# Kernel optimization log

Hardware: AMD Instinct MI355X
Metric: run time of the kernel (lower is better)

The kernel has to match this reference:

```python
import jax, jax.numpy as jnp
import numpy as np

STRIDE = 1
PADDING = 1
THRESHOLD = 0.5
NAN_FRAC = 0.05


def _conv(x, k, stride):
    return jax.lax.conv_general_dilated(
        x, k, (stride, stride), 'VALID',
        dimension_numbers=('NCHW', 'OIHW', 'NCHW'))


def setup_inputs() -> dict:
    key = jax.random.key(0)
    k1, k2, k3, k4 = jax.random.split(key, 4)
    B, C, H, W = 16, 128, 128, 128
    OC, KH, KW = 256, 3, 3
    x = jax.random.normal(k1, (B, C, H, W), jnp.float32)
    nan_mask = jax.random.uniform(k2, (B, C, H, W)) < NAN_FRAC
    x = jnp.where(nan_mask, jnp.nan, x)
    kernel = jax.random.normal(k3, (OC, C, KH, KW), jnp.float32) * 0.05
    bias = jax.random.normal(k4, (OC,), jnp.float32) * 0.05
    return {"x": x, "kernel": kernel, "bias": bias}


def reference(x, kernel, bias):
    # NaN-aware conv: per-patch nan stats shared across out_channels.
    p = PADDING
    x = jnp.pad(x, ((0, 0), (0, 0), (p, p), (p, p)))  # zero pad (zeros are valid values)
    mask = jnp.isnan(x)
    x0 = jnp.where(mask, jnp.zeros((), x.dtype), x)
    OC, C, KH, KW = kernel.shape
    total = float(C * KH * KW)
    ones = jnp.ones((1, C, KH, KW), x.dtype)
    maskf = mask.astype(x.dtype)
    nan_count = _conv(maskf, ones, STRIDE)      # [B,1,oh,ow]
    val_sum = _conv(x0, ones, STRIDE)           # sum of non-nan values per patch
    valid = total - nan_count
    patch_mean = val_sum / jnp.maximum(valid, 1.0)
    s1 = _conv(x0, kernel, STRIDE)              # conv with NaNs zeroed
    m = _conv(maskf, kernel, STRIDE)            # sum of kernel weights at NaN positions
    out = s1 + patch_mean * m + bias[None, :, None, None]
    bad = nan_count / total >= THRESHOLD        # includes all-NaN patches
    return jnp.where(bad, jnp.nan, out)
```

## Files before the change

kernel.cpp:

```cpp
#include <hip/hip_runtime.h>


typedef __attribute__((ext_vector_type(8))) short bf16x8;
typedef __attribute__((ext_vector_type(4))) float f32x4;

#define HH 128
#define WW 128
#define CC 128

__device__ __forceinline__ unsigned short f2bf(float f) {
    union { float f; unsigned int i; } v; v.f = f;
    unsigned int u = v.i;
    if ((u & 0x7FFFFFFFu) > 0x7F800000u) return (unsigned short)((u >> 16) | 0x0040u);
    unsigned int r = u + 0x7FFFu + ((u >> 16) & 1u);
    return (unsigned short)(r >> 16);
}
__device__ __forceinline__ unsigned int sel2(unsigned int v, unsigned int pmu) {
    unsigned int lo = v & 0xFFFFu, hi = v >> 16;
    if ((lo & 0x7FFFu) > 0x7F80u) lo = pmu;
    if ((hi & 0x7FFFu) > 0x7F80u) hi = pmu;
    return lo | (hi << 16);
}
__device__ __forceinline__ void gl16(const void* g, void* l) {
    __builtin_amdgcn_global_load_lds(
        (const __attribute__((address_space(1))) unsigned int*)g,
        (__attribute__((address_space(3))) unsigned int*)l, 16, 0, 0);
}

__global__ void k_transpose_stats(const float* __restrict__ x,
                                  unsigned short* __restrict__ xT,
                                  float* __restrict__ cnt,
                                  float* __restrict__ sum, int b0) {
    int bh = blockIdx.x;
    int bl = bh >> 7, h = bh & 127;
    int b = b0 + bl;
    int w = threadIdx.x;
    const float* xp = x + ((long)b * CC * HH * WW) + h * WW + w;
    unsigned short* xTp = xT + ((((long)bh << 7) + w) << 7);
    int cntv = 0; float sumv = 0.f;
    for (int c8 = 0; c8 < 16; ++c8) {
        unsigned short s8[8];
        #pragma unroll
        for (int j = 0; j < 8; ++j) {
            float fv = xp[(long)(c8 * 8 + j) * (HH * WW)];
            unsigned int bits = __float_as_uint(fv);
            if ((bits & 0x7FFFFFFFu) > 0x7F800000u) { cntv++; s8[j] = 0x7FC0u; }
            else { sumv += fv; s8[j] = f2bf(fv); }
        }
        uint4 p;
        p.x = (unsigned)s8[0] | ((unsigned)s8[1] << 16);
        p.y = (unsigned)s8[2] | ((unsigned)s8[3] << 16);
        p.z = (unsigned)s8[4] | ((unsigned)s8[5] << 16);
        p.w = (unsigned)s8[6] | ((unsigned)s8[7] << 16);
        *(uint4*)(xTp + c8 * 8) = p;
    }
    cnt[(bh << 7) + w] = (float)cntv;
    sum[(bh << 7) + w] = sumv;
}

__global__ void k_patchmean(const float* __restrict__ cnt, const float* __restrict__ sum,
                            unsigned short* __restrict__ pm) {
    int idx = blockIdx.x * 256 + threadIdx.x;
    int ow = idx & 127, oh = (idx >> 7) & 127, bl = idx >> 14;
    float nc = 0.f, vs = 0.f;
    #pragma unroll
    for (int kh = 0; kh < 3; ++kh) {
        int ih = oh + kh - 1; if (ih < 0 || ih >= HH) continue;
        #pragma unroll
        for (int kw = 0; kw < 3; ++kw) {
            int iw = ow + kw - 1; if (iw < 0 || iw >= WW) continue;
            int p = (((bl << 7) + ih) << 7) + iw;
            nc += cnt[p]; vs += sum[p];
        }
    }
    float pmv = vs / fmaxf(1152.f - nc, 1.f);
    unsigned short r = f2bf(pmv);
    if (nc >= 576.f) r = 0x7FC0u;
    pm[idx] = r;
}

__global__ void k_w2(const float* __restrict__ krn, unsigned short* __restrict__ W2) {
    int e = blockIdx.x * 256 + threadIdx.x;
    int s = e & 63;
    int r = (e >> 6) & 255;
    int half = (e >> 14) & 1;
    int khw = e >> 15;
    int c = (half << 6) | (s ^ ((r & 7) << 3));
    W2[e] = f2bf(krn[(r * 128 + c) * 9 + khw]);
}

__global__ __launch_bounds__(256) void k_gemm(
    const unsigned short* __restrict__ xT, const unsigned short* __restrict__ pm,
    const unsigned short* __restrict__ W2, const float* __restrict__ bias,
    float* __restrict__ out, int b0) {
    __shared__ __align__(16) unsigned short lA[2][64 * 64];
    __shared__ __align__(16) unsigned short lB[2][256 * 64];

    int bid = blockIdx.x;
    int ow0 = (bid & 1) << 6;
    int oh  = (bid >> 1) & 127;
    int bl  = bid >> 8;
    int b   = b0 + bl;

    int tid = threadIdx.x;
    int lane = tid & 63, wave = tid >> 6;
    int l15 = lane & 15, quad = lane >> 4;

    int arow = tid >> 2, apart = tid & 3;
    int ow = ow0 + arow;
    unsigned int pmr = pm[(((bl << 7) + oh) << 7) + ow];

    const char* w2base = (const char*)W2;
    int bgoff = (wave << 13) + (lane << 4);
    int bloff = (wave << 13);

    f32x4 acc[4][4];
    #pragma unroll
    for (int i = 0; i < 4; ++i)
        #pragma unroll
        for (int j = 0; j < 4; ++j) acc[i][j] = (f32x4)0.f;

    auto STAGE = [&](unsigned short* la, unsigned short* lb, int s) {
        int khw = s >> 1, c0 = (s & 1) << 6;
        int kh = khw / 3, kw = khw - kh * 3;
        int ih = oh + kh - 1, iw = ow + kw - 1;
        const char* bsrc = w2base + (s << 15) + bgoff;
        char* ldst = (char*)lb + bloff;
        #pragma unroll
        for (int i = 0; i < 8; ++i)
            gl16(bsrc + (i << 10), ldst + (i << 10));
        uint4 v0 = {0u,0u,0u,0u}, v1 = {0u,0u,0u,0u};
        if ((unsigned)ih < 128u && (unsigned)iw < 128u) {
            const unsigned short* ap =
                xT + ((((long)((bl << 7) + ih) << 7) + iw) << 7) + c0 + (apart << 4);
            v0 = *(const uint4*)ap;
            v1 = *(const uint4*)(ap + 8);
        }
        uint4 r0, r1;
        r0.x = sel2(v0.x, pmr); r0.y = sel2(v0.y, pmr);
        r0.z = sel2(v0.z, pmr); r0.w = sel2(v0.w, pmr);
        r1.x = sel2(v1.x, pmr); r1.y = sel2(v1.y, pmr);
        r1.z = sel2(v1.z, pmr); r1.w = sel2(v1.w, pmr);
        char* lar = (char*)la + (arow << 7);
        int sw = (arow & 7) << 4;
        *(uint4*)(lar + (((apart << 5) | 0)  ^ sw)) = r0;
        *(uint4*)(lar + (((apart << 5) | 16) ^ sw)) = r1;
    };

    auto COMPUTE = [&](const unsigned short* la, const unsigned short* lb) {
        int swr = (l15 & 7) << 4;
        #pragma unroll
        for (int ks = 0; ks < 2; ++ks) {
            bf16x8 af[4], bfr[4];
            int cb = ((ks << 6) | (quad << 4)) ^ swr;
            #pragma unroll
            for (int mi = 0; mi < 4; ++mi) {
                int r = (mi << 4) + l15;
                af[mi] = *(const bf16x8*)((const char*)la + (r << 7) + cb);
            }
            #pragma unroll
            for (int ni = 0; ni < 4; ++ni) {
                int r = (wave << 6) + (ni << 4) + l15;
                bfr[ni] = *(const bf16x8*)((const char*)lb + (r << 7) + cb);
            }
            #pragma unroll
            for (int mi = 0; mi < 4; ++mi)
                #pragma unroll
                for (int ni = 0; ni < 4; ++ni)
                    acc[mi][ni] = __builtin_amdgcn_mfma_f32_16x16x32_bf16(
                        af[mi], bfr[ni], acc[mi][ni], 0, 0, 0);
        }
    };

    STAGE(lA[0], lB[0], 0);
    __syncthreads();
    for (int s = 0; s < 18; s += 2) {
        STAGE(lA[1], lB[1], s + 1);
        COMPUTE(lA[0], lB[0]);
        __syncthreads();
        if (s + 2 < 18) STAGE(lA[0], lB[0], s + 2);
        COMPUTE(lA[1], lB[1]);
        __syncthreads();
    }

    #pragma unroll
    for (int ni = 0; ni < 4; ++ni) {
        int oc = (wave << 6) + (ni << 4) + l15;
        float bv = bias[oc];
        float* op = out + ((long)((b << 8) + oc) * 128 + oh) * 128 + ow0;
        #pragma unroll
        for (int mi = 0; mi < 4; ++mi) {
            int og = (mi << 4) + (quad << 2);
            float4 o;
            o.x = acc[mi][ni][0] + bv;
            o.y = acc[mi][ni][1] + bv;
            o.z = acc[mi][ni][2] + bv;
            o.w = acc[mi][ni][3] + bv;
            *(float4*)(op + og) = o;
        }
    }
}

extern "C" void kernel_launch(void* const* d_in, const int* in_sizes, int n_in,
                              void* d_out, int out_size, void* d_ws, size_t ws_size,
                              hipStream_t stream) {
    const float* x    = (const float*)d_in[0];
    const float* krn  = (const float*)d_in[1];
    const float* bias = (const float*)d_in[2];
    float* out = (float*)d_out;

    const size_t W2_BYTES = 294912ull * 2;
    int G = 16;
    while (G > 1) {
        size_t need = W2_BYTES + 256
                    + (size_t)G * (16384ull * 128 * 2)
                    + (size_t)G * (16384ull * 4) * 2
                    + (size_t)G * (16384ull * 2)
                    + 1024;
        if (need <= ws_size) break;
        G >>= 1;
    }

    char* ws = (char*)d_ws;
    size_t off = 0;
    auto carve = [&](size_t bytes) { char* p = ws + off; off += (bytes + 255) & ~255ull; return p; };
    unsigned short* W2  = (unsigned short*)carve(W2_BYTES);
    unsigned short* xT  = (unsigned short*)carve((size_t)G * 16384 * 128 * 2);
    float*          cnt = (float*)carve((size_t)G * 16384 * 4);
    float*          sum = (float*)carve((size_t)G * 16384 * 4);
    unsigned short* pm  = (unsigned short*)carve((size_t)G * 16384 * 2);

    k_w2<<<dim3(1152), dim3(256), 0, stream>>>(krn, W2);
    for (int b0 = 0; b0 < 16; b0 += G) {
        k_transpose_stats<<<dim3(G * 128), dim3(128), 0, stream>>>(x, xT, cnt, sum, b0);
        k_patchmean<<<dim3(G * 64), dim3(256), 0, stream>>>(cnt, sum, pm);
        k_gemm<<<dim3(G * 256), dim3(256), 0, stream>>>(xT, pm, W2, bias, out, b0);
    }
}
```

Baseline: 672.9 us.

## Enlarge GEMM tile to full row, software-pipeline loads, coalesce transpose writes via LDS

```diff
diff --git a/kernel.cpp b/kernel.cpp
--- a/kernel.cpp
+++ b/kernel.cpp
@@ -26,17 +26,18 @@
         (const __attribute__((address_space(1))) unsigned int*)g,
         (__attribute__((address_space(3))) unsigned int*)l, 16, 0, 0);
 }
+#define SBAR() __builtin_amdgcn_sched_barrier(0)
 
 __global__ void k_transpose_stats(const float* __restrict__ x,
                                   unsigned short* __restrict__ xT,
                                   float* __restrict__ cnt,
                                   float* __restrict__ sum, int b0) {
+    __shared__ __align__(16) unsigned short ls[128][136];
     int bh = blockIdx.x;
     int bl = bh >> 7, h = bh & 127;
     int b = b0 + bl;
     int w = threadIdx.x;
     const float* xp = x + ((long)b * CC * HH * WW) + h * WW + w;
-    unsigned short* xTp = xT + ((((long)bh << 7) + w) << 7);
     int cntv = 0; float sumv = 0.f;
     for (int c8 = 0; c8 < 16; ++c8) {
         unsigned short s8[8];
@@ -52,10 +53,18 @@
         p.y = (unsigned)s8[2] | ((unsigned)s8[3] << 16);
         p.z = (unsigned)s8[4] | ((unsigned)s8[5] << 16);
         p.w = (unsigned)s8[6] | ((unsigned)s8[7] << 16);
-        *(uint4*)(xTp + c8 * 8) = p;
+        *(uint4*)&ls[w][c8 * 8] = p;
     }
     cnt[(bh << 7) + w] = (float)cntv;
     sum[(bh << 7) + w] = sumv;
+    __syncthreads();
+    unsigned short* xb = xT + ((long)bh << 14);
+    int ch = w & 15, pw = w >> 4;
+    #pragma unroll
+    for (int r = 0; r < 16; ++r) {
+        int p = (r << 3) + pw;
+        *(uint4*)(xb + (p << 7) + (ch << 3)) = *(const uint4*)&ls[p][ch << 3];
+    }
 }
 
 __global__ void k_patchmean(const float* __restrict__ cnt, const float* __restrict__ sum,
@@ -89,30 +98,28 @@
     W2[e] = f2bf(krn[(r * 128 + c) * 9 + khw]);
 }
 
-__global__ __launch_bounds__(256) void k_gemm(
+__global__ __launch_bounds__(512, 2) void k_gemm(
     const unsigned short* __restrict__ xT, const unsigned short* __restrict__ pm,
     const unsigned short* __restrict__ W2, const float* __restrict__ bias,
     float* __restrict__ out, int b0) {
-    __shared__ __align__(16) unsigned short lA[2][64 * 64];
+    __shared__ __align__(16) unsigned short lA[2][128 * 64];
     __shared__ __align__(16) unsigned short lB[2][256 * 64];
 
     int bid = blockIdx.x;
-    int ow0 = (bid & 1) << 6;
-    int oh  = (bid >> 1) & 127;
-    int bl  = bid >> 8;
-    int b   = b0 + bl;
+    int oh = bid & 127, bl = bid >> 7;
+    int b = b0 + bl;
 
     int tid = threadIdx.x;
     int lane = tid & 63, wave = tid >> 6;
+    int wm = wave >> 2, wn = wave & 3;
     int l15 = lane & 15, quad = lane >> 4;
 
     int arow = tid >> 2, apart = tid & 3;
-    int ow = ow0 + arow;
-    unsigned int pmr = pm[(((bl << 7) + oh) << 7) + ow];
+    unsigned int pmr = pm[(((bl << 7) + oh) << 7) + arow];
 
     const char* w2base = (const char*)W2;
-    int bgoff = (wave << 13) + (lane << 4);
-    int bloff = (wave << 13);
+    int bsrcoff = (wave << 10) + (lane << 4);
+    int bdstoff = (wave << 10);
 
     f32x4 acc[4][4];
     #pragma unroll
@@ -120,22 +127,29 @@
         #pragma unroll
         for (int j = 0; j < 4; ++j) acc[i][j] = (f32x4)0.f;
 
-    auto STAGE = [&](unsigned short* la, unsigned short* lb, int s) {
-        int khw = s >> 1, c0 = (s & 1) << 6;
+    auto issueB = [&](int s, unsigned short* lbbuf) {
+        const char* src = w2base + ((long)s << 15) + bsrcoff;
+        char* dst = (char*)lbbuf + bdstoff;
+        #pragma unroll
+        for (int i = 0; i < 4; ++i)
+            gl16(src + (i << 13), dst + (i << 13));
+    };
+    auto loadA = [&](int s, uint4& v0, uint4& v1, unsigned& msk) {
+        int khw = s >> 1, c0s = (s & 1) << 6;
         int kh = khw / 3, kw = khw - kh * 3;
-        int ih = oh + kh - 1, iw = ow + kw - 1;
-        const char* bsrc = w2base + (s << 15) + bgoff;
-        char* ldst = (char*)lb + bloff;
-        #pragma unroll
-        for (int i = 0; i < 8; ++i)
-            gl16(bsrc + (i << 10), ldst + (i << 10));
-        uint4 v0 = {0u,0u,0u,0u}, v1 = {0u,0u,0u,0u};
-        if ((unsigned)ih < 128u && (unsigned)iw < 128u) {
-            const unsigned short* ap =
-                xT + ((((long)((bl << 7) + ih) << 7) + iw) << 7) + c0 + (apart << 4);
-            v0 = *(const uint4*)ap;
-            v1 = *(const uint4*)(ap + 8);
-        }
+        int ih = oh + kh - 1, iw = arow + kw - 1;
+        bool valid = ((unsigned)ih < 128u) && ((unsigned)iw < 128u);
+        int ihc = ih < 0 ? 0 : (ih > 127 ? 127 : ih);
+        int iwc = iw < 0 ? 0 : (iw > 127 ? 127 : iw);
+        const uint4* ap = (const uint4*)(xT +
+            ((((long)((bl << 7) + ihc) << 7) + iwc) << 7) + c0s + (apart << 4));
+        v0 = ap[0];
+        v1 = ap[1];
+        msk = valid ? 0xFFFFFFFFu : 0u;
+    };
+    auto stageA = [&](uint4 v0, uint4 v1, unsigned msk, unsigned short* la) {
+        v0.x &= msk; v0.y &= msk; v0.z &= msk; v0.w &= msk;
+        v1.x &= msk; v1.y &= msk; v1.z &= msk; v1.w &= msk;
         uint4 r0, r1;
         r0.x = sel2(v0.x, pmr); r0.y = sel2(v0.y, pmr);
         r0.z = sel2(v0.z, pmr); r0.w = sel2(v0.w, pmr);
@@ -146,7 +160,6 @@
         *(uint4*)(lar + (((apart << 5) | 0)  ^ sw)) = r0;
         *(uint4*)(lar + (((apart << 5) | 16) ^ sw)) = r1;
     };
-
     auto COMPUTE = [&](const unsigned short* la, const unsigned short* lb) {
         int swr = (l15 & 7) << 4;
         #pragma unroll
@@ -155,12 +168,12 @@
             int cb = ((ks << 6) | (quad << 4)) ^ swr;
             #pragma unroll
             for (int mi = 0; mi < 4; ++mi) {
-                int r = (mi << 4) + l15;
+                int r = (wm << 6) + (mi << 4) + l15;
                 af[mi] = *(const bf16x8*)((const char*)la + (r << 7) + cb);
             }
             #pragma unroll
             for (int ni = 0; ni < 4; ++ni) {
-                int r = (wave << 6) + (ni << 4) + l15;
+                int r = (wn << 6) + (ni << 4) + l15;
                 bfr[ni] = *(const bf16x8*)((const char*)lb + (r << 7) + cb);
             }
             #pragma unroll
@@ -172,31 +185,52 @@
         }
     };
 
-    STAGE(lA[0], lB[0], 0);
-    __syncthreads();
-    for (int s = 0; s < 18; s += 2) {
-        STAGE(lA[1], lB[1], s + 1);
-        COMPUTE(lA[0], lB[0]);
-        __syncthreads();
-        if (s + 2 < 18) STAGE(lA[0], lB[0], s + 2);
-        COMPUTE(lA[1], lB[1]);
-        __syncthreads();
+    uint4 av0[2], av1[2]; unsigned am[2];
+
+    issueB(0, lB[0]); SBAR();
+    loadA(0, av0[0], av1[0], am[0]); SBAR();
+    loadA(1, av0[1], av1[1], am[1]); SBAR();
+    asm volatile("s_waitcnt vmcnt(2)" ::: "memory");
+    SBAR();
+    stageA(av0[0], av1[0], am[0], lA[0]);
+    asm volatile("s_waitcnt lgkmcnt(0)" ::: "memory");
+    SBAR();
+    __builtin_amdgcn_s_barrier();
+    SBAR();
+
+    #pragma unroll
+    for (int s = 0; s < 18; ++s) {
+        const int cur = s & 1, nxt = cur ^ 1;
+        if (s < 17) { issueB(s + 1, lB[nxt]); SBAR(); }
+        if (s < 16) { loadA(s + 2, av0[cur], av1[cur], am[cur]); SBAR(); }
+        if (s < 16)      { asm volatile("s_waitcnt vmcnt(6)" ::: "memory"); }
+        else if (s == 16){ asm volatile("s_waitcnt vmcnt(4)" ::: "memory"); }
+        SBAR();
+        if (s < 17) stageA(av0[nxt], av1[nxt], am[nxt], lA[nxt]);
+        COMPUTE(lA[cur], lB[cur]);
+        if (s < 17) {
+            if (s < 16) { asm volatile("s_waitcnt vmcnt(2) lgkmcnt(0)" ::: "memory"); }
+            else        { asm volatile("s_waitcnt vmcnt(0) lgkmcnt(0)" ::: "memory"); }
+            SBAR();
+            __builtin_amdgcn_s_barrier();
+            SBAR();
+        }
     }
 
     #pragma unroll
     for (int ni = 0; ni < 4; ++ni) {
-        int oc = (wave << 6) + (ni << 4) + l15;
+        int oc = (wn << 6) + (ni << 4) + l15;
         float bv = bias[oc];
-        float* op = out + ((long)((b << 8) + oc) * 128 + oh) * 128 + ow0;
+        float* op = out + ((long)((b << 8) + oc) * 128 + oh) * 128;
         #pragma unroll
         for (int mi = 0; mi < 4; ++mi) {
-            int og = (mi << 4) + (quad << 2);
+            int ow0 = (wm << 6) + (mi << 4) + (quad << 2);
             float4 o;
             o.x = acc[mi][ni][0] + bv;
             o.y = acc[mi][ni][1] + bv;
             o.z = acc[mi][ni][2] + bv;
             o.w = acc[mi][ni][3] + bv;
-            *(float4*)(op + og) = o;
+            *(float4*)(op + ow0) = o;
         }
     }
 }
@@ -234,6 +268,6 @@
     for (int b0 = 0; b0 < 16; b0 += G) {
         k_transpose_stats<<<dim3(G * 128), dim3(128), 0, stream>>>(x, xT, cnt, sum, b0);
         k_patchmean<<<dim3(G * 64), dim3(256), 0, stream>>>(cnt, sum, pm);
-        k_gemm<<<dim3(G * 256), dim3(256), 0, stream>>>(xT, pm, W2, bias, out, b0);
-    }
-}
+        k_gemm<<<dim3(G * 128), dim3(512), 0, stream>>>(xT, pm, W2, bias, out, b0);
+    }
+}
```

Measured after the change: 657.4 us. 1.02x faster.
